# Kernel optimization log

Measured on AMD Instinct MI355X. Metric: run time of the kernel, lower is better.

The kernel has to match this reference:

```python
import jax, jax.numpy as jnp
import numpy as np

E = float(np.e)

def setup_inputs() -> dict:
    key = jax.random.key(0)
    ks = jax.random.split(key, 6)
    B, T, D, U = 128, 256, 512, 1024
    return {
        "sequences": jax.random.normal(ks[0], (B, T, D), dtype=jnp.float32),
        "time_deltas": jax.random.uniform(ks[1], (B, T), dtype=jnp.float32) * 5.0,
        "kernel": jax.random.normal(ks[2], (D, 3 * U), dtype=jnp.float32) * 0.02,
        "recurrent_kernel": jax.random.normal(ks[3], (U, 3 * U), dtype=jnp.float32) * 0.02,
        "input_bias": jax.random.normal(ks[4], (3 * U,), dtype=jnp.float32) * 0.02,
        "recurrent_bias": jax.random.normal(ks[5], (3 * U,), dtype=jnp.float32) * 0.02,
    }


def reference(sequences, time_deltas, kernel, recurrent_kernel, input_bias, recurrent_bias):
    B, T, D = sequences.shape
    U = recurrent_kernel.shape[0]
    # decay factor per (b, t): 1 / log(e + dt)
    decay = 1.0 / jnp.log(E + time_deltas)  # [B, T]
    # batched input projection for all timesteps (one big GEMM)
    x_proj = jnp.einsum('btd,df->btf', sequences, kernel) + input_bias  # [B, T, 3U]
    x_z, x_r, x_h = jnp.split(x_proj, 3, axis=-1)

    def step(h, xs):
        xz_t, xr_t, xh_t, dec_t = xs
        h_dec = h * dec_t[:, None]  # time-decay modulated state
        rec = h_dec @ recurrent_kernel + recurrent_bias  # [B, 3U]
        r_z, r_r, r_h = jnp.split(rec, 3, axis=-1)
        z = jax.nn.sigmoid(xz_t + r_z)
        r = jax.nn.sigmoid(xr_t + r_r)
        hh = jnp.tanh(xh_t + r * r_h)  # reset_after=True formulation
        h_new = z * h_dec + (1.0 - z) * hh
        return h_new, None

    h0 = jnp.zeros((B, U), dtype=sequences.dtype)
    xs = (
        jnp.swapaxes(x_z, 0, 1),  # [T, B, U]
        jnp.swapaxes(x_r, 0, 1),
        jnp.swapaxes(x_h, 0, 1),
        jnp.swapaxes(decay, 0, 1),  # [T, B]
    )
    h_last, _ = jax.lax.scan(step, h0, xs)
    return h_last  # [B, U]
```

## Files before the change

### kernel.cpp

```cpp
#include <hip/hip_runtime.h>
#include <math.h>

namespace {
constexpr int B_ = 128;
constexpr int T_ = 256;
constexpr int D_ = 512;
constexpr int U_ = 1024;
constexpr int N3U = 3 * U_;
constexpr int K_TOT = D_ + U_;
constexpr int NBG = 4;
constexpr int NUB = 64;
constexpr int WROWS = 48;
constexpr int ROWB = 3088;
constexpr int EXCH_OFF = WROWS * ROWB;
constexpr int LDS_BYTES = EXCH_OFF + 6 * 2048;
constexpr int POLL_LIM = 1 << 20;
}

#define E_CONST 2.71828182845904523536f

using bf16x8 = __attribute__((ext_vector_type(8))) short;
using f32x4  = __attribute__((ext_vector_type(4))) float;

__device__ inline unsigned short f2bf(float f) {
    union { float f; unsigned int u; } a; a.f = f;
    unsigned int u = a.u;
    return (unsigned short)((u + 0x7FFFu + ((u >> 16) & 1u)) >> 16);
}

__device__ inline bf16x8 cvt8(const float* src) {
    float v[8];
    *reinterpret_cast<float4*>(&v[0]) = *reinterpret_cast<const float4*>(src);
    *reinterpret_cast<float4*>(&v[4]) = *reinterpret_cast<const float4*>(src + 4);
    bf16x8 r;
    #pragma unroll
    for (int j = 0; j < 8; ++j) r[j] = (short)f2bf(v[j]);
    return r;
}

#define ISSUE8(arr, base, G)                                                   \
    {                                                                          \
        _Pragma("unroll")                                                      \
        for (int j = 0; j < 8; ++j) {                                          \
            asm volatile("global_load_dwordx4 %0, %1, off offset:%2 sc0 sc1"   \
                         : "=&v"(arr[j])                                       \
                         : "v"(base), "i"((G) * 512 + j * 64));                \
        }                                                                      \
    }

#define PIN8(arr)                                                              \
    {                                                                          \
        _Pragma("unroll")                                                      \
        for (int j = 0; j < 8; ++j) asm volatile("" : "+v"(arr[j]));           \
    }

#define WAITV(N) asm volatile("s_waitcnt vmcnt(" #N ")" ::: "memory")

__global__ void wprep(const float* __restrict__ Wk, const float* __restrict__ Wr,
                      unsigned short* __restrict__ WcatT) {
    __shared__ unsigned short S[32][33];
    const int kb = blockIdx.x * 32;
    const int nb = blockIdx.y * 32;
    const int tx = threadIdx.x;
    const int ty = threadIdx.y;
    #pragma unroll
    for (int j = 0; j < 4; ++j) {
        const int r = ty + 8 * j;
        const int k = kb + r;
        const int n = nb + tx;
        const float v = (k < D_) ? Wk[(size_t)k * N3U + n]
                                 : Wr[(size_t)(k - D_) * N3U + n];
        S[tx][r] = f2bf(v);
    }
    __syncthreads();
    #pragma unroll
    for (int j = 0; j < 4; ++j) {
        const int r = ty + 8 * j;
        WcatT[(size_t)(nb + r) * K_TOT + kb + tx] = S[r][tx];
    }
}

__global__ __launch_bounds__(512) void tgru_flags4(
    const float* __restrict__ seq,
    const float* __restrict__ dts,
    const unsigned short* __restrict__ WcatT,
    const float* __restrict__ ib,
    const float* __restrict__ rb,
    unsigned short* hbA,
    unsigned short* hbB,
    unsigned int* flags,
    float* __restrict__ out)
{
    extern __shared__ char lds[];

    const int tid  = threadIdx.x;
    const int lane = tid & 63;
    const int w    = tid >> 6;
    const int l15  = lane & 15;
    const int lk   = lane >> 4;
    const int bid  = blockIdx.x;
    const int bg   = (bid >> 1) & 3;
    const int ub   = ((bid >> 3) << 1) | (bid & 1);
    const int u0   = ub * 16;

    for (int idx = tid; idx < WROWS * 192; idx += 512) {
        const int c = idx / 192;
        const int o = idx % 192;
        const unsigned short* src =
            WcatT + (size_t)((c >> 4) * U_ + u0 + (c & 15)) * K_TOT + o * 8;
        *reinterpret_cast<bf16x8*>(lds + (size_t)c * ROWB + o * 16) =
            *reinterpret_cast<const bf16x8*>(src);
    }
    __syncthreads();

    float* exf = reinterpret_cast<float*>(lds + EXCH_OFF);

    const int up = lane & 7;
    const int rg = lane >> 3;
    float bzs[2], brs[2], ibh_[2], rbh_[2];
    float hreg[2][2] = {{0.f, 0.f}, {0.f, 0.f}};
    if (w >= 6) {
        #pragma unroll
        for (int f = 0; f < 2; ++f) {
            const int u = u0 + 2 * up + f;
            bzs[f]  = ib[u] + rb[u];
            brs[f]  = ib[U_ + u] + rb[U_ + u];
            ibh_[f] = ib[2 * U_ + u];
            rbh_[f] = rb[2 * U_ + u];
        }
    }
    unsigned int* myflag = flags + ((bg << 6) + ub) * 16 + (w - 6);

    #pragma unroll 1
    for (int t = 0; t < T_; ++t) {
        const unsigned short* hbp = (t & 1) ? hbB : hbA;
        unsigned short*       hbn = (t & 1) ? hbA : hbB;
        float decn[2];

        f32x4 aX = {0.f, 0.f, 0.f, 0.f};
        f32x4 aH = {0.f, 0.f, 0.f, 0.f};
        const char* wrow = lds + (size_t)((w >> 1) * 16 + l15) * ROWB + 16 * lk;
        const int bgemm = bg * 32 + (w & 1) * 16 + l15;

        if (w < 6) {
            const float* ap = seq + ((size_t)bgemm * T_ + t) * D_ + 8 * lk;
            #pragma unroll 8
            for (int ks = 0; ks < 16; ++ks) {
                const bf16x8 a = cvt8(ap + 32 * ks);
                const bf16x8 bf = *reinterpret_cast<const bf16x8*>(wrow + 64 * ks);
                aX = __builtin_amdgcn_mfma_f32_16x16x32_bf16(a, bf, aX, 0, 0, 0);
            }
        } else {
            const int tn = (t < T_ - 1) ? t + 1 : t;
            #pragma unroll
            for (int e = 0; e < 2; ++e) {
                const int b = bg * 32 + (w - 6) * 16 + rg * 2 + e;
                decn[e] = 1.0f / logf(E_CONST + dts[b * T_ + tn]);
            }
            if (w == 7 && t > 0) {
                const unsigned long long* fl =
                    (const unsigned long long*)(flags + ((bg << 6) + lane) * 16);
                int guard = 0;
                for (;;) {
                    const unsigned long long v = __hip_atomic_load(
                        fl, __ATOMIC_RELAXED, __HIP_MEMORY_SCOPE_AGENT);
                    const int ok = ((unsigned)(v & 0xffffffffu) >= (unsigned)t) &&
                                   ((unsigned)(v >> 32)         >= (unsigned)t);
                    if (__all(ok)) break;
                    if (++guard > POLL_LIM) break;
                }
                __builtin_amdgcn_fence(__ATOMIC_ACQUIRE, "workgroup");
            }
        }

        __syncthreads();

        if (w < 6) {
            if (t > 0) {
                const char* hbase =
                    (const char*)(hbp + (size_t)bgemm * U_ + 8 * lk);
                bf16x8 h0[8], h1[8], h2[8], h3[8];
                ISSUE8(h0, hbase, 0)
                ISSUE8(h1, hbase, 1)
                ISSUE8(h2, hbase, 2)
                ISSUE8(h3, hbase, 3)

                WAITV(24); PIN8(h0)
                #pragma unroll
                for (int j = 0; j < 8; ++j) {
                    const bf16x8 bf = *reinterpret_cast<const bf16x8*>(
                        wrow + 1024 + 64 * (0 * 8 + j));
                    aH = __builtin_amdgcn_mfma_f32_16x16x32_bf16(h0[j], bf, aH, 0, 0, 0);
                }
                WAITV(16); PIN8(h1)
                #pragma unroll
                for (int j = 0; j < 8; ++j) {
                    const bf16x8 bf = *reinterpret_cast<const bf16x8*>(
                        wrow + 1024 + 64 * (1 * 8 + j));
                    aH = __builtin_amdgcn_mfma_f32_16x16x32_bf16(h1[j], bf, aH, 0, 0, 0);
                }
                WAITV(8); PIN8(h2)
                #pragma unroll
                for (int j = 0; j < 8; ++j) {
                    const bf16x8 bf = *reinterpret_cast<const bf16x8*>(
                        wrow + 1024 + 64 * (2 * 8 + j));
                    aH = __builtin_amdgcn_mfma_f32_16x16x32_bf16(h2[j], bf, aH, 0, 0, 0);
                }
                WAITV(0); PIN8(h3)
                #pragma unroll
                for (int j = 0; j < 8; ++j) {
                    const bf16x8 bf = *reinterpret_cast<const bf16x8*>(
                        wrow + 1024 + 64 * (3 * 8 + j));
                    aH = __builtin_amdgcn_mfma_f32_16x16x32_bf16(h3[j], bf, aH, 0, 0, 0);
                }
            }
            *reinterpret_cast<f32x4*>(&exf[w * 512 + lane * 4]) = aX;
            *reinterpret_cast<f32x4*>(&exf[w * 512 + 256 + lane * 4]) = aH;
        }

        __syncthreads();

        if (w >= 6) {
            const int bt = w - 6;
            #pragma unroll
            for (int e = 0; e < 2; ++e) {
                const int bl  = rg * 2 + e;
                const int b   = bg * 32 + bt * 16 + bl;
                const int lkq = (bl >> 2) * 16;
                const int q   = bl & 3;
                float hn2[2];
                #pragma unroll
                for (int f = 0; f < 2; ++f) {
                    const int ul = 2 * up + f;
                    const int i0 = (0 * 2 + bt) * 512 + (lkq + ul) * 4 + q;
                    const int i1 = (1 * 2 + bt) * 512 + (lkq + ul) * 4 + q;
                    const int i2 = (2 * 2 + bt) * 512 + (lkq + ul) * 4 + q;
                    const float z  = 1.0f / (1.0f + expf(-(exf[i0] + exf[i0 + 256] + bzs[f])));
                    const float r  = 1.0f / (1.0f + expf(-(exf[i1] + exf[i1 + 256] + brs[f])));
                    const float hh = tanhf(exf[i2] + ibh_[f] + r * (exf[i2 + 256] + rbh_[f]));
                    hn2[f] = z * hreg[e][f] + (1.0f - z) * hh;
                }
                if (t == T_ - 1) {
                    *reinterpret_cast<float2*>(&out[(size_t)b * U_ + u0 + 2 * up]) =
                        make_float2(hn2[0], hn2[1]);
                } else {
                    const float hd0 = hn2[0] * decn[e];
                    const float hd1 = hn2[1] * decn[e];
                    hreg[e][0] = hd0;
                    hreg[e][1] = hd1;
                    const unsigned int pk =
                        (unsigned int)f2bf(hd0) | ((unsigned int)f2bf(hd1) << 16);
                    __hip_atomic_store(
                        reinterpret_cast<unsigned int*>(&hbn[(size_t)b * U_ + u0 + 2 * up]),
                        pk, __ATOMIC_RELAXED, __HIP_MEMORY_SCOPE_AGENT);
                }
            }
            if (t < T_ - 1) {
                asm volatile("s_waitcnt vmcnt(0)" ::: "memory");
                if (lane == 0) {
                    __hip_atomic_store(myflag, (unsigned int)(t + 1),
                                       __ATOMIC_RELAXED, __HIP_MEMORY_SCOPE_AGENT);
                }
            }
        }
    }
}

extern "C" void kernel_launch(void* const* d_in, const int* in_sizes, int n_in,
                              void* d_out, int out_size, void* d_ws, size_t ws_size,
                              hipStream_t stream) {
    const float* seq = (const float*)d_in[0];
    const float* dts = (const float*)d_in[1];
    const float* Wk  = (const float*)d_in[2];
    const float* Wr  = (const float*)d_in[3];
    const float* ib  = (const float*)d_in[4];
    const float* rb  = (const float*)d_in[5];
    float* out = (float*)d_out;

    char* wsb = (char*)d_ws;
    unsigned short* wcat = (unsigned short*)(wsb);
    unsigned short* hbA  = (unsigned short*)(wsb + 9437184);
    unsigned short* hbB  = (unsigned short*)(wsb + 9699328);
    unsigned int*   flags = (unsigned int*)(wsb + 9961472);

    hipMemsetAsync(flags, 0, 16384, stream);

    wprep<<<dim3(K_TOT / 32, N3U / 32), dim3(32, 8), 0, stream>>>(Wk, Wr, wcat);

    hipFuncSetAttribute((const void*)tgru_flags4,
                        hipFuncAttributeMaxDynamicSharedMemorySize, LDS_BYTES);

    void* args[] = {
        (void*)&seq, (void*)&dts, (void*)&wcat, (void*)&ib, (void*)&rb,
        (void*)&hbA, (void*)&hbB, (void*)&flags, (void*)&out
    };
    hipLaunchCooperativeKernel((void*)tgru_flags4, dim3(NBG * NUB), dim3(512),
                               args, LDS_BYTES, stream);
}
```

Baseline: 3.166 ms.

## Restructure GRU recurrence into per-wave batch chains without block barriers

Replaces the 256-block cooperative kernel, which split GEMM and gate work across waves with LDS exchange and two block barriers per step, with 64 blocks of 4 waves. Each wave handles 32 batch rows for all three gates of a 16-unit slice and synchronizes only with the matching waves in other blocks through per-wave flags. Decay factors are precomputed by a separate kernel. The aim is to cut barrier and exchange latency on the serial critical path. In exchange it runs on far fewer CUs, so each wave does more MFMA work per step. It also drops the cooperative launch, which risks deadlock if the 64 blocks are not all co-resident.

```diff
diff --git a/kernel.cpp b/kernel.cpp
--- a/kernel.cpp
+++ b/kernel.cpp
@@ -8,12 +8,11 @@
 constexpr int U_ = 1024;
 constexpr int N3U = 3 * U_;
 constexpr int K_TOT = D_ + U_;
-constexpr int NBG = 4;
-constexpr int NUB = 64;
+constexpr int NBLK = 64;
+constexpr int NW = 4;
 constexpr int WROWS = 48;
 constexpr int ROWB = 3088;
-constexpr int EXCH_OFF = WROWS * ROWB;
-constexpr int LDS_BYTES = EXCH_OFF + 6 * 2048;
+constexpr int LDS_BYTES = WROWS * ROWB;
 constexpr int POLL_LIM = 1 << 20;
 }
 
@@ -80,9 +79,14 @@
     }
 }
 
-__global__ __launch_bounds__(512) void tgru_flags4(
+__global__ void dprep(const float* __restrict__ dts, float* __restrict__ decays) {
+    const int i = blockIdx.x * 256 + threadIdx.x;
+    if (i < B_ * T_) decays[i] = 1.0f / logf(E_CONST + dts[i]);
+}
+
+__global__ __launch_bounds__(256) void tgru_chains(
     const float* __restrict__ seq,
-    const float* __restrict__ dts,
+    const float* __restrict__ decays,
     const unsigned short* __restrict__ WcatT,
     const float* __restrict__ ib,
     const float* __restrict__ rb,
@@ -98,12 +102,11 @@
     const int w    = tid >> 6;
     const int l15  = lane & 15;
     const int lk   = lane >> 4;
-    const int bid  = blockIdx.x;
-    const int bg   = (bid >> 1) & 3;
-    const int ub   = ((bid >> 3) << 1) | (bid & 1);
+    const int ub   = blockIdx.x;
     const int u0   = ub * 16;
-
-    for (int idx = tid; idx < WROWS * 192; idx += 512) {
+    const int u    = u0 + l15;
+
+    for (int idx = tid; idx < WROWS * 192; idx += 256) {
         const int c = idx / 192;
         const int o = idx % 192;
         const unsigned short* src =
@@ -113,72 +116,60 @@
     }
     __syncthreads();
 
-    float* exf = reinterpret_cast<float*>(lds + EXCH_OFF);
-
-    const int up = lane & 7;
-    const int rg = lane >> 3;
-    float bzs[2], brs[2], ibh_[2], rbh_[2];
-    float hreg[2][2] = {{0.f, 0.f}, {0.f, 0.f}};
-    if (w >= 6) {
-        #pragma unroll
-        for (int f = 0; f < 2; ++f) {
-            const int u = u0 + 2 * up + f;
-            bzs[f]  = ib[u] + rb[u];
-            brs[f]  = ib[U_ + u] + rb[U_ + u];
-            ibh_[f] = ib[2 * U_ + u];
-            rbh_[f] = rb[2 * U_ + u];
-        }
-    }
-    unsigned int* myflag = flags + ((bg << 6) + ub) * 16 + (w - 6);
+    const char* wz = lds + (size_t)(0  + l15) * ROWB + 16 * lk;
+    const char* wr = lds + (size_t)(16 + l15) * ROWB + 16 * lk;
+    const char* wh = lds + (size_t)(32 + l15) * ROWB + 16 * lk;
+
+    const float bzs  = ib[u] + rb[u];
+    const float brs  = ib[U_ + u] + rb[U_ + u];
+    const float ibh_ = ib[2 * U_ + u];
+    const float rbh_ = rb[2 * U_ + u];
+
+    float hreg[2][4] = {{0.f,0.f,0.f,0.f},{0.f,0.f,0.f,0.f}};
+    unsigned int* myflag = flags + (w * 64 + ub) * 16;
+    const unsigned int* pollp = flags + (w * 64 + lane) * 16;
 
     #pragma unroll 1
     for (int t = 0; t < T_; ++t) {
         const unsigned short* hbp = (t & 1) ? hbB : hbA;
         unsigned short*       hbn = (t & 1) ? hbA : hbB;
-        float decn[2];
-
-        f32x4 aX = {0.f, 0.f, 0.f, 0.f};
-        f32x4 aH = {0.f, 0.f, 0.f, 0.f};
-        const char* wrow = lds + (size_t)((w >> 1) * 16 + l15) * ROWB + 16 * lk;
-        const int bgemm = bg * 32 + (w & 1) * 16 + l15;
-
-        if (w < 6) {
-            const float* ap = seq + ((size_t)bgemm * T_ + t) * D_ + 8 * lk;
-            #pragma unroll 8
+
+        f32x4 az[2], ar[2], ahx[2], ahr[2];
+        #pragma unroll
+        for (int bt = 0; bt < 2; ++bt) {
+            az[bt] = {0.f,0.f,0.f,0.f}; ar[bt] = {0.f,0.f,0.f,0.f};
+            ahx[bt] = {0.f,0.f,0.f,0.f}; ahr[bt] = {0.f,0.f,0.f,0.f};
+        }
+
+        #pragma unroll
+        for (int bt = 0; bt < 2; ++bt) {
+            const int b = 32 * w + 16 * bt + l15;
+            const float* ap = seq + ((size_t)b * T_ + t) * D_ + 8 * lk;
+            #pragma unroll 4
             for (int ks = 0; ks < 16; ++ks) {
                 const bf16x8 a = cvt8(ap + 32 * ks);
-                const bf16x8 bf = *reinterpret_cast<const bf16x8*>(wrow + 64 * ks);
-                aX = __builtin_amdgcn_mfma_f32_16x16x32_bf16(a, bf, aX, 0, 0, 0);
-            }
-        } else {
-            const int tn = (t < T_ - 1) ? t + 1 : t;
+                az[bt]  = __builtin_amdgcn_mfma_f32_16x16x32_bf16(
+                    a, *reinterpret_cast<const bf16x8*>(wz + 64 * ks), az[bt], 0, 0, 0);
+                ar[bt]  = __builtin_amdgcn_mfma_f32_16x16x32_bf16(
+                    a, *reinterpret_cast<const bf16x8*>(wr + 64 * ks), ar[bt], 0, 0, 0);
+                ahx[bt] = __builtin_amdgcn_mfma_f32_16x16x32_bf16(
+                    a, *reinterpret_cast<const bf16x8*>(wh + 64 * ks), ahx[bt], 0, 0, 0);
+            }
+        }
+
+        if (t > 0) {
+            int guard = 0;
+            for (;;) {
+                const unsigned int v = __hip_atomic_load(
+                    pollp, __ATOMIC_RELAXED, __HIP_MEMORY_SCOPE_AGENT);
+                if (__all((int)(v >= (unsigned int)t))) break;
+                if (++guard > POLL_LIM) break;
+            }
+
             #pragma unroll
-            for (int e = 0; e < 2; ++e) {
-                const int b = bg * 32 + (w - 6) * 16 + rg * 2 + e;
-                decn[e] = 1.0f / logf(E_CONST + dts[b * T_ + tn]);
-            }
-            if (w == 7 && t > 0) {
-                const unsigned long long* fl =
-                    (const unsigned long long*)(flags + ((bg << 6) + lane) * 16);
-                int guard = 0;
-                for (;;) {
-                    const unsigned long long v = __hip_atomic_load(
-                        fl, __ATOMIC_RELAXED, __HIP_MEMORY_SCOPE_AGENT);
-                    const int ok = ((unsigned)(v & 0xffffffffu) >= (unsigned)t) &&
-                                   ((unsigned)(v >> 32)         >= (unsigned)t);
-                    if (__all(ok)) break;
-                    if (++guard > POLL_LIM) break;
-                }
-                __builtin_amdgcn_fence(__ATOMIC_ACQUIRE, "workgroup");
-            }
-        }
-
-        __syncthreads();
-
-        if (w < 6) {
-            if (t > 0) {
-                const char* hbase =
-                    (const char*)(hbp + (size_t)bgemm * U_ + 8 * lk);
+            for (int bt = 0; bt < 2; ++bt) {
+                const int b = 32 * w + 16 * bt + l15;
+                const char* hbase = (const char*)(hbp + (size_t)b * U_ + 8 * lk);
                 bf16x8 h0[8], h1[8], h2[8], h3[8];
                 ISSUE8(h0, hbase, 0)
                 ISSUE8(h1, hbase, 1)
@@ -188,79 +179,75 @@
                 WAITV(24); PIN8(h0)
                 #pragma unroll
                 for (int j = 0; j < 8; ++j) {
-                    const bf16x8 bf = *reinterpret_cast<const bf16x8*>(
-                        wrow + 1024 + 64 * (0 * 8 + j));
-                    aH = __builtin_amdgcn_mfma_f32_16x16x32_bf16(h0[j], bf, aH, 0, 0, 0);
+                    const int o = 1024 + 64 * (0 * 8 + j);
+                    az[bt]  = __builtin_amdgcn_mfma_f32_16x16x32_bf16(
+                        h0[j], *reinterpret_cast<const bf16x8*>(wz + o), az[bt], 0, 0, 0);
+                    ar[bt]  = __builtin_amdgcn_mfma_f32_16x16x32_bf16(
+                        h0[j], *reinterpret_cast<const bf16x8*>(wr + o), ar[bt], 0, 0, 0);
+                    ahr[bt] = __builtin_amdgcn_mfma_f32_16x16x32_bf16(
+                        h0[j], *reinterpret_cast<const bf16x8*>(wh + o), ahr[bt], 0, 0, 0);
                 }
                 WAITV(16); PIN8(h1)
                 #pragma unroll
                 for (int j = 0; j < 8; ++j) {
-                    const bf16x8 bf = *reinterpret_cast<const bf16x8*>(
-                        wrow + 1024 + 64 * (1 * 8 + j));
-                    aH = __builtin_amdgcn_mfma_f32_16x16x32_bf16(h1[j], bf, aH, 0, 0, 0);
+                    const int o = 1024 + 64 * (1 * 8 + j);
+                    az[bt]  = __builtin_amdgcn_mfma_f32_16x16x32_bf16(
+                        h1[j], *reinterpret_cast<const bf16x8*>(wz + o), az[bt], 0, 0, 0);
+                    ar[bt]  = __builtin_amdgcn_mfma_f32_16x16x32_bf16(
+                        h1[j], *reinterpret_cast<const bf16x8*>(wr + o), ar[bt], 0, 0, 0);
+                    ahr[bt] = __builtin_amdgcn_mfma_f32_16x16x32_bf16(
+                        h1[j], *reinterpret_cast<const bf16x8*>(wh + o), ahr[bt], 0, 0, 0);
                 }
                 WAITV(8); PIN8(h2)
                 #pragma unroll
                 for (int j = 0; j < 8; ++j) {
-                    const bf16x8 bf = *reinterpret_cast<const bf16x8*>(
-                        wrow + 1024 + 64 * (2 * 8 + j));
-                    aH = __builtin_amdgcn_mfma_f32_16x16x32_bf16(h2[j], bf, aH, 0, 0, 0);
+                    const int o = 1024 + 64 * (2 * 8 + j);
+                    az[bt]  = __builtin_amdgcn_mfma_f32_16x16x32_bf16(
+                        h2[j], *reinterpret_cast<const bf16x8*>(wz + o), az[bt], 0, 0, 0);
+                    ar[bt]  = __builtin_amdgcn_mfma_f32_16x16x32_bf16(
+                        h2[j], *reinterpret_cast<const bf16x8*>(wr + o), ar[bt], 0, 0, 0);
+                    ahr[bt] = __builtin_amdgcn_mfma_f32_16x16x32_bf16(
+                        h2[j], *reinterpret_cast<const bf16x8*>(wh + o), ahr[bt], 0, 0, 0);
                 }
                 WAITV(0); PIN8(h3)
                 #pragma unroll
                 for (int j = 0; j < 8; ++j) {
-                    const bf16x8 bf = *reinterpret_cast<const bf16x8*>(
-                        wrow + 1024 + 64 * (3 * 8 + j));
-                    aH = __builtin_amdgcn_mfma_f32_16x16x32_bf16(h3[j], bf, aH, 0, 0, 0);
-                }
-            }
-            *reinterpret_cast<f32x4*>(&exf[w * 512 + lane * 4]) = aX;
-            *reinterpret_cast<f32x4*>(&exf[w * 512 + 256 + lane * 4]) = aH;
-        }
-
-        __syncthreads();
-
-        if (w >= 6) {
-            const int bt = w - 6;
+                    const int o = 1024 + 64 * (3 * 8 + j);
+                    az[bt]  = __builtin_amdgcn_mfma_f32_16x16x32_bf16(
+                        h3[j], *reinterpret_cast<const bf16x8*>(wz + o), az[bt], 0, 0, 0);
+                    ar[bt]  = __builtin_amdgcn_mfma_f32_16x16x32_bf16(
+                        h3[j], *reinterpret_cast<const bf16x8*>(wr + o), ar[bt], 0, 0, 0);
+                    ahr[bt] = __builtin_amdgcn_mfma_f32_16x16x32_bf16(
+                        h3[j], *reinterpret_cast<const bf16x8*>(wh + o), ahr[bt], 0, 0, 0);
+                }
+            }
+        }
+
+        #pragma unroll
+        for (int bt = 0; bt < 2; ++bt) {
             #pragma unroll
-            for (int e = 0; e < 2; ++e) {
-                const int bl  = rg * 2 + e;
-                const int b   = bg * 32 + bt * 16 + bl;
-                const int lkq = (bl >> 2) * 16;
-                const int q   = bl & 3;
-                float hn2[2];
-                #pragma unroll
-                for (int f = 0; f < 2; ++f) {
-                    const int ul = 2 * up + f;
-                    const int i0 = (0 * 2 + bt) * 512 + (lkq + ul) * 4 + q;
-                    const int i1 = (1 * 2 + bt) * 512 + (lkq + ul) * 4 + q;
-                    const int i2 = (2 * 2 + bt) * 512 + (lkq + ul) * 4 + q;
-                    const float z  = 1.0f / (1.0f + expf(-(exf[i0] + exf[i0 + 256] + bzs[f])));
-                    const float r  = 1.0f / (1.0f + expf(-(exf[i1] + exf[i1 + 256] + brs[f])));
-                    const float hh = tanhf(exf[i2] + ibh_[f] + r * (exf[i2 + 256] + rbh_[f]));
-                    hn2[f] = z * hreg[e][f] + (1.0f - z) * hh;
-                }
+            for (int q = 0; q < 4; ++q) {
+                const int b = 32 * w + 16 * bt + 4 * lk + q;
+                const float z  = 1.0f / (1.0f + expf(-(az[bt][q] + bzs)));
+                const float r  = 1.0f / (1.0f + expf(-(ar[bt][q] + brs)));
+                const float hh = tanhf(ahx[bt][q] + ibh_ + r * (ahr[bt][q] + rbh_));
+                const float hn = z * hreg[bt][q] + (1.0f - z) * hh;
                 if (t == T_ - 1) {
-                    *reinterpret_cast<float2*>(&out[(size_t)b * U_ + u0 + 2 * up]) =
-                        make_float2(hn2[0], hn2[1]);
+                    out[(size_t)b * U_ + u] = hn;
                 } else {
-                    const float hd0 = hn2[0] * decn[e];
-                    const float hd1 = hn2[1] * decn[e];
-                    hreg[e][0] = hd0;
-                    hreg[e][1] = hd1;
-                    const unsigned int pk =
-                        (unsigned int)f2bf(hd0) | ((unsigned int)f2bf(hd1) << 16);
-                    __hip_atomic_store(
-                        reinterpret_cast<unsigned int*>(&hbn[(size_t)b * U_ + u0 + 2 * up]),
-                        pk, __ATOMIC_RELAXED, __HIP_MEMORY_SCOPE_AGENT);
-                }
-            }
-            if (t < T_ - 1) {
-                asm volatile("s_waitcnt vmcnt(0)" ::: "memory");
-                if (lane == 0) {
-                    __hip_atomic_store(myflag, (unsigned int)(t + 1),
+                    const float hd = hn * decays[b * T_ + t + 1];
+                    hreg[bt][q] = hd;
+                    __hip_atomic_store(&hbn[(size_t)b * U_ + u], f2bf(hd),
                                        __ATOMIC_RELAXED, __HIP_MEMORY_SCOPE_AGENT);
                 }
+            }
+        }
+
+        if (t < T_ - 1) {
+            WAITV(0);
+            if (lane == 0) {
+                __hip_atomic_store(myflag, (unsigned int)(t + 1),
+                                   __ATOMIC_RELAXED, __HIP_MEMORY_SCOPE_AGENT);
             }
         }
     }
@@ -278,22 +265,20 @@
     float* out = (float*)d_out;
 
     char* wsb = (char*)d_ws;
-    unsigned short* wcat = (unsigned short*)(wsb);
-    unsigned short* hbA  = (unsigned short*)(wsb + 9437184);
-    unsigned short* hbB  = (unsigned short*)(wsb + 9699328);
-    unsigned int*   flags = (unsigned int*)(wsb + 9961472);
+    unsigned short* wcat  = (unsigned short*)(wsb);
+    float*          decays = (float*)(wsb + 9437184);
+    unsigned short* hbA   = (unsigned short*)(wsb + 9568256);
+    unsigned short* hbB   = (unsigned short*)(wsb + 9830400);
+    unsigned int*   flags = (unsigned int*)(wsb + 10092544);
 
     hipMemsetAsync(flags, 0, 16384, stream);
 
     wprep<<<dim3(K_TOT / 32, N3U / 32), dim3(32, 8), 0, stream>>>(Wk, Wr, wcat);
-
-    hipFuncSetAttribute((const void*)tgru_flags4,
+    dprep<<<dim3((B_ * T_ + 255) / 256), dim3(256), 0, stream>>>(dts, decays);
+
+    hipFuncSetAttribute((const void*)tgru_chains,
                         hipFuncAttributeMaxDynamicSharedMemorySize, LDS_BYTES);
 
-    void* args[] = {
-        (void*)&seq, (void*)&dts, (void*)&wcat, (void*)&ib, (void*)&rb,
-        (void*)&hbA, (void*)&hbB, (void*)&flags, (void*)&out
-    };
-    hipLaunchCooperativeKernel((void*)tgru_flags4, dim3(NBG * NUB), dim3(512),
-                               args, LDS_BYTES, stream);
-}
+    tgru_chains<<<dim3(NBLK), dim3(256), LDS_BYTES, stream>>>(
+        seq, decays, wcat, ib, rb, hbA, hbB, flags, out);
+}
```

Result: slower. 7.033 ms (+122.2%).
